# Kernel tuning notes

Hardware: AMD Instinct MI355X
Metric: run time of the kernel (lower is better)

Reference implementation:

```python
import jax, jax.numpy as jnp
import numpy as np

RATIO = 0.25
LN_EPS = 1e-5
D_IN = 512
D_OUT = 512


def setup_inputs() -> dict:
    key = jax.random.key(0)
    ks = jax.random.split(key, 8)
    B, N = 8, 16384
    features = jax.random.normal(ks[0], (B, N, D_IN), dtype=jnp.float32)
    coords = jax.random.uniform(ks[1], (B, N, 2), dtype=jnp.float32)
    times = jax.random.uniform(ks[2], (B, N), dtype=jnp.float32)
    polarities = jax.random.uniform(ks[3], (B, N), dtype=jnp.float32)
    # learned params: nn.Linear(D_IN, D_OUT) + nn.LayerNorm(D_OUT)
    W = jax.random.normal(ks[4], (D_OUT, D_IN), dtype=jnp.float32) / np.sqrt(D_IN)
    b = jnp.zeros((D_OUT,), dtype=jnp.float32)
    gamma = jnp.ones((D_OUT,), dtype=jnp.float32)
    beta = jnp.zeros((D_OUT,), dtype=jnp.float32)
    return {"features": features, "coords": coords, "times": times,
            "polarities": polarities, "W": W, "b": b, "gamma": gamma, "beta": beta}


def farthest_point_sample(coords, times, num_samples):
    # coords [B,N,2], times [B,N] -> indices [B,num_samples]
    B, N, _ = coords.shape
    points = jnp.concatenate([coords, times[..., None]], axis=-1)  # [B,N,3]
    first = jnp.zeros((B,), dtype=jnp.int32)  # deterministic seed point (torch uses randint)
    dist0 = jnp.full((B, N), jnp.inf, dtype=points.dtype)
    barange = jnp.arange(B)

    def step(carry, _):
        dist_min, last = carry
        last_pt = points[barange, last]                         # [B,3]
        d = jnp.sqrt(jnp.sum((points - last_pt[:, None, :]) ** 2, axis=-1) + 1e-8)
        dist_min = jnp.minimum(dist_min, d)                     # [B,N]
        nxt = jnp.argmax(dist_min, axis=-1).astype(jnp.int32)   # [B]
        return (dist_min, nxt), nxt

    (_, _), rest = jax.lax.scan(step, (dist0, first), None, length=num_samples - 1)
    # rest: [num_samples-1, B] -> [B, num_samples]
    return jnp.concatenate([first[:, None], rest.T], axis=1)


def layer_norm(x, gamma, beta):
    mu = jnp.mean(x, axis=-1, keepdims=True)
    var = jnp.mean((x - mu) ** 2, axis=-1, keepdims=True)
    return (x - mu) * jax.lax.rsqrt(var + LN_EPS) * gamma + beta


def reference(features, coords, times, polarities, W, b, gamma, beta):
    B, N, _ = features.shape
    M = max(int(N * RATIO), 1)
    idx = farthest_point_sample(coords, times, M)               # [B,M]
    feats_out = jnp.take_along_axis(features, idx[..., None], axis=1)   # [B,M,D_in]
    coords_out = jnp.take_along_axis(coords, idx[..., None], axis=1)    # [B,M,2]
    times_out = jnp.take_along_axis(times, idx, axis=1)                 # [B,M]
    pol_out = jnp.take_along_axis(polarities, idx, axis=1)              # [B,M]
    proj = jnp.einsum('bmd,od->bmo', feats_out, W) + b                  # [B,M,D_out]
    feats_out = layer_norm(proj, gamma, beta)
    return feats_out, coords_out, times_out, pol_out
```

## Files before the change

### kernel.cpp

```cpp
#include <hip/hip_runtime.h>
#include <math.h>

#define B_ 8
#define N_ 16384
#define M_ 4096
#define D_ 512
#define TPB 1024
#define PPT 16

#define FEAT_SZ (B_ * M_ * D_)
#define COFF FEAT_SZ
#define TOFF (FEAT_SZ + 2 * B_ * M_)
#define POFF (TOFF + B_ * M_)

#define R16(F) F(0) F(1) F(2) F(3) F(4) F(5) F(6) F(7) \
               F(8) F(9) F(10) F(11) F(12) F(13) F(14) F(15)

template <int CTRL>
__device__ __forceinline__ float dpp_max_step(float x) {
    const int y = __builtin_amdgcn_update_dpp(0, __float_as_int(x),
                                              CTRL, 0xf, 0xf, true);
    return fmaxf(x, __int_as_float(y));
}

__device__ __forceinline__ unsigned spread4(unsigned v) {
    return (v & 1u) | ((v & 2u) << 2) | ((v & 4u) << 4) | ((v & 8u) << 6);
}
__device__ __forceinline__ unsigned mcode(float x, float y, float tt) {
    unsigned mx = min((unsigned)(int)(x * 16.0f), 15u);
    unsigned my = min((unsigned)(int)(y * 16.0f), 15u);
    unsigned mt = min((unsigned)(int)(tt * 16.0f), 15u);
    return spread4(mx) | (spread4(my) << 1) | (spread4(mt) << 2);
}

__global__ __launch_bounds__(TPB) void msort_kernel(
    const float* __restrict__ coords, const float* __restrict__ times,
    float* __restrict__ sortx, float* __restrict__ sorty,
    float* __restrict__ sortt, unsigned* __restrict__ sortid)
{
    const int b = blockIdx.x, t = threadIdx.x;
    const float* cb = coords + (size_t)b * N_ * 2;
    const float* tb = times + (size_t)b * N_;
    const size_t bo = (size_t)b * N_;

    __shared__ unsigned cnt[4096];
    __shared__ unsigned wsum[TPB];

    for (int i = t; i < 4096; i += TPB) cnt[i] = 0;
    __syncthreads();

    for (int j = 0; j < PPT; ++j) {
        const int gi = j * TPB + t;
        const float2 c2 = *(const float2*)(cb + 2 * (size_t)gi);
        atomicAdd(&cnt[mcode(c2.x, c2.y, tb[gi])], 1u);
    }
    __syncthreads();

    {
        const unsigned c0 = cnt[4 * t], c1 = cnt[4 * t + 1],
                       c2 = cnt[4 * t + 2], c3 = cnt[4 * t + 3];
        wsum[t] = c0 + c1 + c2 + c3;
        __syncthreads();
        if (t == 0) {
            unsigned run = 0;
            for (int i = 0; i < TPB; ++i) { unsigned v = wsum[i]; wsum[i] = run; run += v; }
        }
        __syncthreads();
        const unsigned base = wsum[t];
        cnt[4 * t] = base;
        cnt[4 * t + 1] = base + c0;
        cnt[4 * t + 2] = base + c0 + c1;
        cnt[4 * t + 3] = base + c0 + c1 + c2;
    }
    __syncthreads();

    for (int j = 0; j < PPT; ++j) {
        const int gi = j * TPB + t;
        const float2 c2 = *(const float2*)(cb + 2 * (size_t)gi);
        const float tt = tb[gi];
        const unsigned pos = atomicAdd(&cnt[mcode(c2.x, c2.y, tt)], 1u);
        sortx[bo + pos] = c2.x;
        sorty[bo + pos] = c2.y;
        sortt[bo + pos] = tt;
        sortid[bo + pos] = (unsigned)gi;
    }
}

__global__ __launch_bounds__(TPB)
__attribute__((amdgpu_waves_per_eu(4, 4)))
void fps_kernel(
    const float* __restrict__ coords, const float* __restrict__ times,
    const float* __restrict__ sortx, const float* __restrict__ sorty,
    const float* __restrict__ sortt, const unsigned* __restrict__ sortid,
    int* __restrict__ idx_out)
{
    const int b = blockIdx.x;
    const int t = threadIdx.x;
    const float* cb = coords + (size_t)b * N_ * 2;
    const float* tb = times + (size_t)b * N_;
    const size_t bo = (size_t)b * N_;

    __shared__ float2 cxy[N_];
    __shared__ __align__(16) float red_s[16];
    __shared__ unsigned long long nxt_pos[2], nxt_t[2];

#define DECLV(i) float pt##i, m##i;
    R16(DECLV)
#undef DECLV
    unsigned id2_0, id2_1, id2_2, id2_3, id2_4, id2_5, id2_6, id2_7;

    float bx0 = 1e30f, bx1 = -1e30f, by0 = 1e30f, by1 = -1e30f,
          bt0 = 1e30f, bt1 = -1e30f;

#define LOADV(i) { const int p = t * PPT + (i);                               \
        const float x = sortx[bo + p], y = sorty[bo + p], tt = sortt[bo + p]; \
        float2 v2; v2.x = x; v2.y = y;                                        \
        cxy[(i) * TPB + t] = v2;                                              \
        pt##i = tt; m##i = INFINITY;                                          \
        bx0 = fminf(bx0, x); bx1 = fmaxf(bx1, x);                             \
        by0 = fminf(by0, y); by1 = fmaxf(by1, y);                             \
        bt0 = fminf(bt0, tt); bt1 = fmaxf(bt1, tt); }
    R16(LOADV)
#undef LOADV

#define LOADID(r) id2_##r = (sortid[bo + t * PPT + 2 * (r)] & 0xffffu) |      \
                            (sortid[bo + t * PPT + 2 * (r) + 1] << 16);
    LOADID(0) LOADID(1) LOADID(2) LOADID(3)
    LOADID(4) LOADID(5) LOADID(6) LOADID(7)
#undef LOADID

#define PINV(i) asm("" : "+v"(pt##i));
    R16(PINV)
#undef PINV
    asm("" : "+v"(id2_0), "+v"(id2_1), "+v"(id2_2), "+v"(id2_3));
    asm("" : "+v"(id2_4), "+v"(id2_5), "+v"(id2_6), "+v"(id2_7));

    if (t == 0) {
        idx_out[b * M_] = 0;
        nxt_pos[0] = nxt_pos[1] = ~0ull;
        nxt_t[0] = nxt_t[1] = ~0ull;
    }
    float lx = cb[0], ly = cb[1], lt = tb[0];
    float TM = INFINITY;
    __syncthreads();

    const int wave = t >> 6;
    const int lane = t & 63;

    for (int k = 1; k < M_; ++k) {
        const int par = k & 1;

        const float ddx = fmaxf(fmaxf(bx0 - lx, lx - bx1), 0.0f);
        const float ddy = fmaxf(fmaxf(by0 - ly, ly - by1), 0.0f);
        const float ddt = fmaxf(fmaxf(bt0 - lt, lt - bt1), 0.0f);
        const float lb2 = __fmaf_rn(ddt, ddt,
                          __fmaf_rn(ddx, ddx, __fmul_rn(ddy, ddy)));

        if (!(lb2 * 0.999996f >= TM)) {
#define UPDV(i) { const float2 c2 = cxy[(i) * TPB + t];                       \
            const float dx = c2.x - lx;                                       \
            const float dy = c2.y - ly;                                       \
            const float dz = pt##i - lt;                                      \
            const float d2 = __fmaf_rn(dz, dz, __fmaf_rn(dx, dx,              \
                                                     __fmul_rn(dy, dy)));     \
            m##i = fminf(m##i, d2); }
            R16(UPDV)
#undef UPDV
            const float a0 = fmaxf(fmaxf(m0, m1), m2);
            const float a1 = fmaxf(fmaxf(m3, m4), m5);
            const float a2 = fmaxf(fmaxf(m6, m7), m8);
            const float a3 = fmaxf(fmaxf(m9, m10), m11);
            const float a4 = fmaxf(fmaxf(m12, m13), m14);
            TM = fmaxf(fmaxf(fmaxf(a0, a1), a2), fmaxf(fmaxf(a3, a4), m15));
        }

        const float s_local = __fsqrt_rn(__fadd_rn(TM, 1e-8f));

        float v = s_local;
        v = dpp_max_step<0x111>(v);
        v = dpp_max_step<0x112>(v);
        v = dpp_max_step<0x114>(v);
        v = dpp_max_step<0x118>(v);
        v = dpp_max_step<0x142>(v);
        v = dpp_max_step<0x143>(v);
        if (lane == 63) red_s[wave] = v;
        __syncthreads();

        if (t == 0) { nxt_pos[par ^ 1] = ~0ull; nxt_t[par ^ 1] = ~0ull; }

        const float4* rp = (const float4*)red_s;
        const float4 r0 = rp[0], r1 = rp[1], r2 = rp[2], r3 = rp[3];
        const float s_star = fmaxf(
            fmaxf(fmaxf(fmaxf(r0.x, r0.y), fmaxf(r0.z, r0.w)),
                  fmaxf(fmaxf(r1.x, r1.y), fmaxf(r1.z, r1.w))),
            fmaxf(fmaxf(fmaxf(r2.x, r2.y), fmaxf(r2.z, r2.w)),
                  fmaxf(fmaxf(r3.x, r3.y), fmaxf(r3.z, r3.w))));

        if (s_local == s_star) {
            const float bm = TM;
            unsigned bid = 0xffffffffu; unsigned bpos = 0; float bt_ = 0.0f;

#define SEL1(j, reg, sh) if (m##j == bm) {                                    \
            const unsigned idj = ((reg) >> (sh)) & 0xffffu;                   \
            if (idj < bid) { bid = idj; bpos = (unsigned)(t * PPT + (j));     \
                             bt_ = pt##j; } }
            SEL1(0, id2_0, 0)  SEL1(1, id2_0, 16)
            SEL1(2, id2_1, 0)  SEL1(3, id2_1, 16)
            SEL1(4, id2_2, 0)  SEL1(5, id2_2, 16)
            SEL1(6, id2_3, 0)  SEL1(7, id2_3, 16)
            SEL1(8, id2_4, 0)  SEL1(9, id2_4, 16)
            SEL1(10, id2_5, 0) SEL1(11, id2_5, 16)
            SEL1(12, id2_6, 0) SEL1(13, id2_6, 16)
            SEL1(14, id2_7, 0) SEL1(15, id2_7, 16)
#undef SEL1

            const unsigned bmu = __float_as_uint(bm);
            const float thresh = __uint_as_float(bmu >= 32u ? bmu - 32u : 0u);
            float cntw = 0.0f;
#define CNTV(i) cntw += (m##i >= thresh) ? 1.0f : 0.0f;
            R16(CNTV)
#undef CNTV
            if (cntw > 1.5f) {
                bid = 0xffffffffu; bpos = 0; bt_ = 0.0f;
#define FIX1(j, reg, sh) if (m##j >= thresh) {                                \
                const float sj = __fsqrt_rn(__fadd_rn(m##j, 1e-8f));          \
                if (sj == s_local) {                                          \
                    const unsigned idj = ((reg) >> (sh)) & 0xffffu;           \
                    if (idj < bid) { bid = idj;                               \
                        bpos = (unsigned)(t * PPT + (j)); bt_ = pt##j; } } }
                FIX1(0, id2_0, 0)  FIX1(1, id2_0, 16)
                FIX1(2, id2_1, 0)  FIX1(3, id2_1, 16)
                FIX1(4, id2_2, 0)  FIX1(5, id2_2, 16)
                FIX1(6, id2_3, 0)  FIX1(7, id2_3, 16)
                FIX1(8, id2_4, 0)  FIX1(9, id2_4, 16)
                FIX1(10, id2_5, 0) FIX1(11, id2_5, 16)
                FIX1(12, id2_6, 0) FIX1(13, id2_6, 16)
                FIX1(14, id2_7, 0) FIX1(15, id2_7, 16)
#undef FIX1
            }
            const unsigned long long hi = ((unsigned long long)bid) << 32;
            atomicMin(&nxt_pos[par], hi | bpos);
            atomicMin(&nxt_t[par], hi | __float_as_uint(bt_));
        }
        __syncthreads();

        const unsigned long long kp = nxt_pos[par];
        const unsigned long long kt = nxt_t[par];
        const int gi = (int)(kp >> 32);
        const unsigned pos = (unsigned)kp;
        lt = __uint_as_float((unsigned)kt);
        const float2 wv = cxy[(pos & 15u) * TPB + (pos >> 4)];
        lx = wv.x; ly = wv.y;
        if (t == 0) idx_out[b * M_ + k] = gi;
    }
}

__global__ __launch_bounds__(256) void gather_kernel(
    const float* __restrict__ coords, const float* __restrict__ times,
    const float* __restrict__ pol, const int* __restrict__ idx,
    float* __restrict__ out)
{
    int i = blockIdx.x * 256 + threadIdx.x;
    if (i >= B_ * M_) return;
    int b = i >> 12;
    int g = b * N_ + idx[i];
    float2 c2 = *(const float2*)(coords + 2 * (size_t)g);
    *(float2*)(out + COFF + 2 * (size_t)i) = c2;
    out[TOFF + i] = times[g];
    out[POFF + i] = pol[g];
}

#define BM 32
#define BN 128
#define BK 32

__global__ __launch_bounds__(256) void proj_kernel(
    const float* __restrict__ features, const float* __restrict__ W,
    const float* __restrict__ bias, const int* __restrict__ idx,
    float* __restrict__ out)
{
    __shared__ float a_lds[BK][BM + 4];
    __shared__ float w_lds[BK][BN];
    __shared__ int   src[BM];

    const int t = threadIdx.x;
    const int rowBase = blockIdx.x * BM;
    const int oBase = blockIdx.y * BN;

    if (t < BM) {
        int row = rowBase + t;
        int b = row >> 12;
        src[t] = b * N_ + idx[row];
    }
    __syncthreads();

    const int rt = t >> 5;
    const int ot = t & 31;
    const int lr = t >> 3;
    const int lk = (t & 7) * 4;

    float c[4][4] = {};

    for (int kc = 0; kc < D_; kc += BK) {
        {
            float4 v = *(const float4*)(features + (size_t)src[lr] * D_ + kc + lk);
            a_lds[lk + 0][lr] = v.x; a_lds[lk + 1][lr] = v.y;
            a_lds[lk + 2][lr] = v.z; a_lds[lk + 3][lr] = v.w;
        }
#pragma unroll
        for (int p = 0; p < 4; ++p) {
            int o = p * 32 + lr;
            float4 v = *(const float4*)(W + (size_t)(oBase + o) * D_ + kc + lk);
            w_lds[lk + 0][o] = v.x; w_lds[lk + 1][o] = v.y;
            w_lds[lk + 2][o] = v.z; w_lds[lk + 3][o] = v.w;
        }
        __syncthreads();

#pragma unroll
        for (int k = 0; k < BK; ++k) {
            float4 af = *(const float4*)&a_lds[k][rt * 4];
            float4 wf = *(const float4*)&w_lds[k][ot * 4];
            float av[4] = { af.x, af.y, af.z, af.w };
            float wv[4] = { wf.x, wf.y, wf.z, wf.w };
#pragma unroll
            for (int ri = 0; ri < 4; ++ri)
#pragma unroll
                for (int oi = 0; oi < 4; ++oi)
                    c[ri][oi] = fmaf(av[ri], wv[oi], c[ri][oi]);
        }
        __syncthreads();
    }

    float4 bv = *(const float4*)(bias + oBase + ot * 4);
    float bvv[4] = { bv.x, bv.y, bv.z, bv.w };
#pragma unroll
    for (int ri = 0; ri < 4; ++ri) {
        int row = rowBase + rt * 4 + ri;
        float4 o4;
        o4.x = c[ri][0] + bvv[0];
        o4.y = c[ri][1] + bvv[1];
        o4.z = c[ri][2] + bvv[2];
        o4.w = c[ri][3] + bvv[3];
        *(float4*)(out + (size_t)row * D_ + oBase + ot * 4) = o4;
    }
}

__global__ __launch_bounds__(256) void ln_kernel(
    float* __restrict__ out, const float* __restrict__ gamma,
    const float* __restrict__ beta)
{
    const int w = threadIdx.x >> 6;
    const int lane = threadIdx.x & 63;
    const size_t row = (size_t)blockIdx.x * 4 + w;
    float* p = out + row * D_;

    float4 v0 = *(const float4*)(p + lane * 8);
    float4 v1 = *(const float4*)(p + lane * 8 + 4);
    float x[8] = { v0.x, v0.y, v0.z, v0.w, v1.x, v1.y, v1.z, v1.w };

    float sum = 0.f;
#pragma unroll
    for (int i = 0; i < 8; ++i) sum += x[i];
#pragma unroll
    for (int off = 1; off < 64; off <<= 1) sum += __shfl_xor(sum, off);
    const float mu = sum * (1.0f / 512.0f);

    float sq = 0.f;
#pragma unroll
    for (int i = 0; i < 8; ++i) { float d = x[i] - mu; sq = fmaf(d, d, sq); }
#pragma unroll
    for (int off = 1; off < 64; off <<= 1) sq += __shfl_xor(sq, off);
    const float inv = rsqrtf(sq * (1.0f / 512.0f) + 1e-5f);

    float4 g0 = *(const float4*)(gamma + lane * 8);
    float4 g1 = *(const float4*)(gamma + lane * 8 + 4);
    float4 b0 = *(const float4*)(beta + lane * 8);
    float4 b1 = *(const float4*)(beta + lane * 8 + 4);
    float g[8] = { g0.x, g0.y, g0.z, g0.w, g1.x, g1.y, g1.z, g1.w };
    float be[8] = { b0.x, b0.y, b0.z, b0.w, b1.x, b1.y, b1.z, b1.w };

    float y[8];
#pragma unroll
    for (int i = 0; i < 8; ++i) y[i] = fmaf((x[i] - mu) * inv, g[i], be[i]);

    float4 o0 = { y[0], y[1], y[2], y[3] };
    float4 o1 = { y[4], y[5], y[6], y[7] };
    *(float4*)(p + lane * 8) = o0;
    *(float4*)(p + lane * 8 + 4) = o1;
}

extern "C" void kernel_launch(void* const* d_in, const int* in_sizes, int n_in,
                              void* d_out, int out_size, void* d_ws, size_t ws_size,
                              hipStream_t stream)
{
    const float* features   = (const float*)d_in[0];
    const float* coords     = (const float*)d_in[1];
    const float* times      = (const float*)d_in[2];
    const float* polarities = (const float*)d_in[3];
    const float* W          = (const float*)d_in[4];
    const float* bias       = (const float*)d_in[5];
    const float* gamma      = (const float*)d_in[6];
    const float* beta       = (const float*)d_in[7];
    float* out = (float*)d_out;

    int* idx = (int*)d_ws;
    float* sortx = (float*)((char*)d_ws + (size_t)B_ * M_ * 4);
    float* sorty = sortx + (size_t)B_ * N_;
    float* sortt = sorty + (size_t)B_ * N_;
    unsigned* sortid = (unsigned*)(sortt + (size_t)B_ * N_);

    msort_kernel<<<B_, TPB, 0, stream>>>(coords, times, sortx, sorty, sortt, sortid);

    fps_kernel<<<B_, TPB, 0, stream>>>(coords, times, sortx, sorty, sortt,
                                       sortid, idx);

    gather_kernel<<<(B_ * M_ + 255) / 256, 256, 0, stream>>>(
        coords, times, polarities, idx, out);

    dim3 pgrid(B_ * M_ / BM, D_ / BN);
    proj_kernel<<<pgrid, 256, 0, stream>>>(features, W, bias, idx, out);

    ln_kernel<<<B_ * M_ / 4, 256, 0, stream>>>(out, gamma, beta);
}
```

Measured before the change: 6.516 ms.

## Replace two-barrier FPS argmax with packed-key single-barrier shuffle reduction

The per-iteration farthest-point selection used two block barriers: a DPP max of the distance, then a shared atomicMin on index keys. It now packs sqrt-distance, the inverted original index and the sorted position into one 64-bit key. Each wave reduces that key with xor shuffles, and all threads scan the 16 per-wave entries after a single barrier, using double-buffered shared slots. Per-thread and per-wave keys are cached and recomputed only when a thread's minimum distances changed, which removes a barrier and the atomics per step at the cost of 64-bit shuffles.

```diff
diff --git a/kernel.cpp b/kernel.cpp
--- a/kernel.cpp
+++ b/kernel.cpp
@@ -15,13 +15,6 @@
 
 #define R16(F) F(0) F(1) F(2) F(3) F(4) F(5) F(6) F(7) \
                F(8) F(9) F(10) F(11) F(12) F(13) F(14) F(15)
-
-template <int CTRL>
-__device__ __forceinline__ float dpp_max_step(float x) {
-    const int y = __builtin_amdgcn_update_dpp(0, __float_as_int(x),
-                                              CTRL, 0xf, 0xf, true);
-    return fmaxf(x, __int_as_float(y));
-}
 
 __device__ __forceinline__ unsigned spread4(unsigned v) {
     return (v & 1u) | ((v & 2u) << 2) | ((v & 4u) << 4) | ((v & 8u) << 6);
@@ -101,8 +94,7 @@
     const size_t bo = (size_t)b * N_;
 
     __shared__ float2 cxy[N_];
-    __shared__ __align__(16) float red_s[16];
-    __shared__ unsigned long long nxt_pos[2], nxt_t[2];
+    __shared__ __align__(16) ulonglong2 red[2][16];
 
 #define DECLV(i) float pt##i, m##i;
     R16(DECLV)
@@ -135,13 +127,13 @@
     asm("" : "+v"(id2_0), "+v"(id2_1), "+v"(id2_2), "+v"(id2_3));
     asm("" : "+v"(id2_4), "+v"(id2_5), "+v"(id2_6), "+v"(id2_7));
 
-    if (t == 0) {
-        idx_out[b * M_] = 0;
-        nxt_pos[0] = nxt_pos[1] = ~0ull;
-        nxt_t[0] = nxt_t[1] = ~0ull;
-    }
+    if (t == 0) idx_out[b * M_] = 0;
     float lx = cb[0], ly = cb[1], lt = tb[0];
     float TM = INFINITY;
+    unsigned long long skey = 0ull;
+    float sbt = 0.0f;
+    unsigned long long wkey = 0ull;
+    float wbt = 0.0f;
     __syncthreads();
 
     const int wave = t >> 6;
@@ -155,8 +147,9 @@
         const float ddt = fmaxf(fmaxf(bt0 - lt, lt - bt1), 0.0f);
         const float lb2 = __fmaf_rn(ddt, ddt,
                           __fmaf_rn(ddx, ddx, __fmul_rn(ddy, ddy)));
-
-        if (!(lb2 * 0.999996f >= TM)) {
+        const bool upd = !(lb2 * 0.999996f >= TM);
+
+        if (upd) {
 #define UPDV(i) { const float2 c2 = cxy[(i) * TPB + t];                       \
             const float dx = c2.x - lx;                                       \
             const float dy = c2.y - ly;                                       \
@@ -172,35 +165,11 @@
             const float a3 = fmaxf(fmaxf(m9, m10), m11);
             const float a4 = fmaxf(fmaxf(m12, m13), m14);
             TM = fmaxf(fmaxf(fmaxf(a0, a1), a2), fmaxf(fmaxf(a3, a4), m15));
-        }
-
-        const float s_local = __fsqrt_rn(__fadd_rn(TM, 1e-8f));
-
-        float v = s_local;
-        v = dpp_max_step<0x111>(v);
-        v = dpp_max_step<0x112>(v);
-        v = dpp_max_step<0x114>(v);
-        v = dpp_max_step<0x118>(v);
-        v = dpp_max_step<0x142>(v);
-        v = dpp_max_step<0x143>(v);
-        if (lane == 63) red_s[wave] = v;
-        __syncthreads();
-
-        if (t == 0) { nxt_pos[par ^ 1] = ~0ull; nxt_t[par ^ 1] = ~0ull; }
-
-        const float4* rp = (const float4*)red_s;
-        const float4 r0 = rp[0], r1 = rp[1], r2 = rp[2], r3 = rp[3];
-        const float s_star = fmaxf(
-            fmaxf(fmaxf(fmaxf(r0.x, r0.y), fmaxf(r0.z, r0.w)),
-                  fmaxf(fmaxf(r1.x, r1.y), fmaxf(r1.z, r1.w))),
-            fmaxf(fmaxf(fmaxf(r2.x, r2.y), fmaxf(r2.z, r2.w)),
-                  fmaxf(fmaxf(r3.x, r3.y), fmaxf(r3.z, r3.w))));
-
-        if (s_local == s_star) {
-            const float bm = TM;
+
+            const float s_local = __fsqrt_rn(__fadd_rn(TM, 1e-8f));
+
             unsigned bid = 0xffffffffu; unsigned bpos = 0; float bt_ = 0.0f;
-
-#define SEL1(j, reg, sh) if (m##j == bm) {                                    \
+#define SEL1(j, reg, sh) if (m##j == TM) {                                    \
             const unsigned idj = ((reg) >> (sh)) & 0xffffu;                   \
             if (idj < bid) { bid = idj; bpos = (unsigned)(t * PPT + (j));     \
                              bt_ = pt##j; } }
@@ -214,8 +183,8 @@
             SEL1(14, id2_7, 0) SEL1(15, id2_7, 16)
 #undef SEL1
 
-            const unsigned bmu = __float_as_uint(bm);
-            const float thresh = __uint_as_float(bmu >= 32u ? bmu - 32u : 0u);
+            const unsigned tmu = __float_as_uint(TM);
+            const float thresh = __uint_as_float(tmu >= 32u ? tmu - 32u : 0u);
             float cntw = 0.0f;
 #define CNTV(i) cntw += (m##i >= thresh) ? 1.0f : 0.0f;
             R16(CNTV)
@@ -238,17 +207,40 @@
                 FIX1(14, id2_7, 0) FIX1(15, id2_7, 16)
 #undef FIX1
             }
-            const unsigned long long hi = ((unsigned long long)bid) << 32;
-            atomicMin(&nxt_pos[par], hi | bpos);
-            atomicMin(&nxt_t[par], hi | __float_as_uint(bt_));
+            skey = (((unsigned long long)__float_as_uint(s_local)) << 32) |
+                   (((unsigned long long)(unsigned)(N_ - 1 - (int)bid)) << 14) |
+                   (unsigned long long)bpos;
+            sbt = bt_;
+        }
+
+        if (__any(upd)) {
+            unsigned long long kk = skey; float tt2 = sbt;
+#pragma unroll
+            for (int off = 1; off < 64; off <<= 1) {
+                const unsigned long long ok = __shfl_xor(kk, off);
+                const float ot = __shfl_xor(tt2, off);
+                if (ok > kk) { kk = ok; tt2 = ot; }
+            }
+            wkey = kk; wbt = tt2;
+        }
+        if (lane == 0) {
+            ulonglong2 wv2;
+            wv2.x = wkey;
+            wv2.y = (unsigned long long)__float_as_uint(wbt);
+            red[par][wave] = wv2;
         }
         __syncthreads();
 
-        const unsigned long long kp = nxt_pos[par];
-        const unsigned long long kt = nxt_t[par];
-        const int gi = (int)(kp >> 32);
-        const unsigned pos = (unsigned)kp;
-        lt = __uint_as_float((unsigned)kt);
+        const ulonglong2* rp = &red[par][0];
+        ulonglong2 best = rp[0];
+#pragma unroll
+        for (int w = 1; w < 16; ++w) {
+            const ulonglong2 o = rp[w];
+            if (o.x > best.x) best = o;
+        }
+        const unsigned pos = (unsigned)(best.x & 0x3fffu);
+        const int gi = N_ - 1 - (int)((best.x >> 14) & 0x3fffu);
+        lt = __uint_as_float((unsigned)best.y);
         const float2 wv = cxy[(pos & 15u) * TPB + (pos >> 4)];
         lx = wv.x; ly = wv.y;
         if (t == 0) idx_out[b * M_ + k] = gi;
```

New measurement: 10.06 ms. 1.54x slower.

## Pack FPS winner into one atomic key and precompute selection before barrier

Applied to the files above, without the earlier changes.

The per-iteration argmax now packs the winner's original index, sorted position and time into a single 64-bit key. One atomicMin replaces the two separate atomics on two shared arrays. Each thread now computes and caches its local candidate key right after updating its minimum distances, before the reduction barrier, and reuses it when the bounding-box test skips the update. This removes the serial selection work that ran between the two barriers on the critical path. In exchange, every updating thread now runs the selection logic each iteration instead of only the winning thread.

```diff
diff --git a/kernel.cpp b/kernel.cpp
--- a/kernel.cpp
+++ b/kernel.cpp
@@ -102,7 +102,7 @@
 
     __shared__ float2 cxy[N_];
     __shared__ __align__(16) float red_s[16];
-    __shared__ unsigned long long nxt_pos[2], nxt_t[2];
+    __shared__ unsigned long long nxt[2];
 
 #define DECLV(i) float pt##i, m##i;
     R16(DECLV)
@@ -137,11 +137,12 @@
 
     if (t == 0) {
         idx_out[b * M_] = 0;
-        nxt_pos[0] = nxt_pos[1] = ~0ull;
-        nxt_t[0] = nxt_t[1] = ~0ull;
+        nxt[0] = ~0ull; nxt[1] = ~0ull;
     }
     float lx = cb[0], ly = cb[1], lt = tb[0];
     float TM = INFINITY;
+    float s_local = 0.0f;
+    unsigned long long skey = ~0ull;
     __syncthreads();
 
     const int wave = t >> 6;
@@ -172,35 +173,11 @@
             const float a3 = fmaxf(fmaxf(m9, m10), m11);
             const float a4 = fmaxf(fmaxf(m12, m13), m14);
             TM = fmaxf(fmaxf(fmaxf(a0, a1), a2), fmaxf(fmaxf(a3, a4), m15));
-        }
-
-        const float s_local = __fsqrt_rn(__fadd_rn(TM, 1e-8f));
-
-        float v = s_local;
-        v = dpp_max_step<0x111>(v);
-        v = dpp_max_step<0x112>(v);
-        v = dpp_max_step<0x114>(v);
-        v = dpp_max_step<0x118>(v);
-        v = dpp_max_step<0x142>(v);
-        v = dpp_max_step<0x143>(v);
-        if (lane == 63) red_s[wave] = v;
-        __syncthreads();
-
-        if (t == 0) { nxt_pos[par ^ 1] = ~0ull; nxt_t[par ^ 1] = ~0ull; }
-
-        const float4* rp = (const float4*)red_s;
-        const float4 r0 = rp[0], r1 = rp[1], r2 = rp[2], r3 = rp[3];
-        const float s_star = fmaxf(
-            fmaxf(fmaxf(fmaxf(r0.x, r0.y), fmaxf(r0.z, r0.w)),
-                  fmaxf(fmaxf(r1.x, r1.y), fmaxf(r1.z, r1.w))),
-            fmaxf(fmaxf(fmaxf(r2.x, r2.y), fmaxf(r2.z, r2.w)),
-                  fmaxf(fmaxf(r3.x, r3.y), fmaxf(r3.z, r3.w))));
-
-        if (s_local == s_star) {
-            const float bm = TM;
+
+            s_local = __fsqrt_rn(__fadd_rn(TM, 1e-8f));
+
             unsigned bid = 0xffffffffu; unsigned bpos = 0; float bt_ = 0.0f;
-
-#define SEL1(j, reg, sh) if (m##j == bm) {                                    \
+#define SEL1(j, reg, sh) if (m##j == TM) {                                    \
             const unsigned idj = ((reg) >> (sh)) & 0xffffu;                   \
             if (idj < bid) { bid = idj; bpos = (unsigned)(t * PPT + (j));     \
                              bt_ = pt##j; } }
@@ -214,8 +191,8 @@
             SEL1(14, id2_7, 0) SEL1(15, id2_7, 16)
 #undef SEL1
 
-            const unsigned bmu = __float_as_uint(bm);
-            const float thresh = __uint_as_float(bmu >= 32u ? bmu - 32u : 0u);
+            const unsigned tmu = __float_as_uint(TM);
+            const float thresh = __uint_as_float(tmu >= 32u ? tmu - 32u : 0u);
             float cntw = 0.0f;
 #define CNTV(i) cntw += (m##i >= thresh) ? 1.0f : 0.0f;
             R16(CNTV)
@@ -238,17 +215,38 @@
                 FIX1(14, id2_7, 0) FIX1(15, id2_7, 16)
 #undef FIX1
             }
-            const unsigned long long hi = ((unsigned long long)bid) << 32;
-            atomicMin(&nxt_pos[par], hi | bpos);
-            atomicMin(&nxt_t[par], hi | __float_as_uint(bt_));
+            skey = (((unsigned long long)bid) << 46) |
+                   (((unsigned long long)bpos) << 32) |
+                   (unsigned long long)__float_as_uint(bt_);
         }
-        __syncthreads();
-
-        const unsigned long long kp = nxt_pos[par];
-        const unsigned long long kt = nxt_t[par];
-        const int gi = (int)(kp >> 32);
-        const unsigned pos = (unsigned)kp;
-        lt = __uint_as_float((unsigned)kt);
+
+        float v = s_local;
+        v = dpp_max_step<0x111>(v);
+        v = dpp_max_step<0x112>(v);
+        v = dpp_max_step<0x114>(v);
+        v = dpp_max_step<0x118>(v);
+        v = dpp_max_step<0x142>(v);
+        v = dpp_max_step<0x143>(v);
+        if (lane == 63) red_s[wave] = v;
+        __syncthreads();
+
+        if (t == 0) nxt[par ^ 1] = ~0ull;
+
+        const float4* rp = (const float4*)red_s;
+        const float4 r0 = rp[0], r1 = rp[1], r2 = rp[2], r3 = rp[3];
+        const float s_star = fmaxf(
+            fmaxf(fmaxf(fmaxf(r0.x, r0.y), fmaxf(r0.z, r0.w)),
+                  fmaxf(fmaxf(r1.x, r1.y), fmaxf(r1.z, r1.w))),
+            fmaxf(fmaxf(fmaxf(r2.x, r2.y), fmaxf(r2.z, r2.w)),
+                  fmaxf(fmaxf(r3.x, r3.y), fmaxf(r3.z, r3.w))));
+
+        if (s_local == s_star) atomicMin(&nxt[par], skey);
+        __syncthreads();
+
+        const unsigned long long wk = nxt[par];
+        const int gi = (int)(wk >> 46);
+        const unsigned pos = (unsigned)(wk >> 32) & 0x3fffu;
+        lt = __uint_as_float((unsigned)wk);
         const float2 wv = cxy[(pos & 15u) * TPB + (pos >> 4)];
         lx = wv.x; ly = wv.y;
         if (t == 0) idx_out[b * M_ + k] = gi;
```

Result: slower. 7.490 ms (+15.0%).
